# Kernel optimization log

Measured on AMD Instinct MI355X. Metric: run time of the kernel, lower is better.

The kernel has to match this reference:

```python
import jax, jax.numpy as jnp
import numpy as np

DIM = 1024
DIM_HEAD = 128
HEADS = 8
DIM_INNER = DIM_HEAD * HEADS


def setup_inputs() -> dict:
    key = jax.random.key(0)
    k_x, k_qkv, k_out = jax.random.split(key, 3)
    x = jax.random.normal(k_x, (2, 2048, DIM), dtype=jnp.float32)
    gamma = jnp.ones((DIM,), dtype=jnp.float32)
    # nn.Linear weights stored as [out, in]; init ~ U(-1/sqrt(in), 1/sqrt(in))
    w_qkv = jax.random.uniform(k_qkv, (DIM_INNER * 3, DIM), dtype=jnp.float32,
                               minval=-1.0, maxval=1.0) / np.sqrt(DIM)
    w_out = jax.random.uniform(k_out, (DIM, DIM_INNER), dtype=jnp.float32,
                               minval=-1.0, maxval=1.0) / np.sqrt(DIM_INNER)
    return {"x": x, "gamma": gamma, "w_qkv": w_qkv, "w_out": w_out}


def reference(x, gamma, w_qkv, w_out):
    scale_norm = DIM ** 0.5
    scale_attn = DIM_HEAD ** -0.5
    # RMSNorm as written: F.normalize (L2) * sqrt(dim) * gamma
    l2 = jnp.sqrt(jnp.sum(x * x, axis=-1, keepdims=True))
    xn = x / jnp.maximum(l2, 1e-12) * scale_norm * gamma
    # QKV projection: [b, n, 3*h*d]
    qkv = jnp.einsum('bnc,fc->bnf', xn, w_qkv)
    b, n, _ = qkv.shape
    qkv = qkv.reshape(b, n, 3, HEADS, DIM_HEAD)
    q, k, v = (qkv[:, :, 0], qkv[:, :, 1], qkv[:, :, 2])  # [b, n, h, d]
    q = q * scale_attn
    sim = jnp.einsum('bihd,bjhd->bhij', q, k)
    causal_mask = jnp.triu(jnp.ones((n, n), dtype=bool), k=1)
    neg = -jnp.finfo(sim.dtype).max
    sim = jnp.where(causal_mask, neg, sim)
    attn = jax.nn.softmax(sim, axis=-1)
    out = jnp.einsum('bhij,bjhd->bihd', attn, v)
    out = out.reshape(b, n, DIM_INNER)  # merge heads: b n (h d)
    return jnp.einsum('bnf,cf->bnc', out, w_out)
```

## Files before the change

kernel.cpp:

```cpp
#include <hip/hip_runtime.h>

#define SEQ 2048
#define NTOK 4096
#define DIM 1024
#define FQKV 3072
#define SC_Q (0.08838834764831843f * 1.4426950408889634f)
#define SC_NORM 32.0f

typedef short short8 __attribute__((ext_vector_type(8)));
typedef float f32x4 __attribute__((ext_vector_type(4)));
typedef float f32x16 __attribute__((ext_vector_type(16)));
typedef unsigned short u16x4 __attribute__((ext_vector_type(4)));

__device__ __forceinline__ unsigned short f2bf(float f) {
    unsigned int u = __float_as_uint(f);
    u += 0x7fffu + ((u >> 16) & 1u);
    return (unsigned short)(u >> 16);
}
__device__ __forceinline__ float bf2f(unsigned short b) {
    return __uint_as_float(((unsigned int)b) << 16);
}
__device__ __forceinline__ void gl_lds16(const void* g, void* l) {
    __builtin_amdgcn_global_load_lds((const __attribute__((address_space(1))) void*)g,
                                     (__attribute__((address_space(3))) void*)l, 16, 0, 0);
}

__global__ __launch_bounds__(256) void prep(const float* __restrict__ x,
                                            const float* __restrict__ gamma,
                                            unsigned short* __restrict__ xn,
                                            const float* __restrict__ wq,
                                            unsigned short* __restrict__ wqb,
                                            const float* __restrict__ wo,
                                            unsigned short* __restrict__ wob) {
    if (blockIdx.x < 4096) {
        int token = blockIdx.x;
        float4 v = ((const float4*)(x + (size_t)token * DIM))[threadIdx.x];
        float ss = v.x * v.x + v.y * v.y + v.z * v.z + v.w * v.w;
#pragma unroll
        for (int off = 32; off > 0; off >>= 1) ss += __shfl_down(ss, off);
        __shared__ float wsum[4];
        if ((threadIdx.x & 63) == 0) wsum[threadIdx.x >> 6] = ss;
        __syncthreads();
        float tot = wsum[0] + wsum[1] + wsum[2] + wsum[3];
        float sc = SC_NORM / fmaxf(sqrtf(tot), 1e-12f);
        float4 g = ((const float4*)gamma)[threadIdx.x];
        u16x4 o;
        o.x = f2bf(v.x * sc * g.x);
        o.y = f2bf(v.y * sc * g.y);
        o.z = f2bf(v.z * sc * g.z);
        o.w = f2bf(v.w * sc * g.w);
        ((u16x4*)(xn + (size_t)token * DIM))[threadIdx.x] = o;
    } else {
        int i = (blockIdx.x - 4096) * 256 + threadIdx.x;
        const float* w; unsigned short* o; int idx;
        if (i < 786432) { w = wq; o = wqb; idx = i; }
        else            { w = wo; o = wob; idx = i - 786432; }
        float4 v = ((const float4*)w)[idx];
        u16x4 r;
        r.x = f2bf(v.x); r.y = f2bf(v.y); r.z = f2bf(v.z); r.w = f2bf(v.w);
        ((u16x4*)o)[idx] = r;
    }
}

template<int C_MODE, int TM>
__global__ __launch_bounds__(256) void gemm_bf16(const unsigned short* __restrict__ A,
                                                 const unsigned short* __restrict__ B,
                                                 void* __restrict__ Cv,
                                                 int M, int N, int K) {
    constexpr int MF = TM / 32;
    __shared__ unsigned short As[TM * 64];
    __shared__ unsigned short Bs[128 * 64];

    int lin = blockIdx.y * gridDim.x + blockIdx.x;
    int nwg = gridDim.x * gridDim.y;
    int w = (lin & 7) * (nwg >> 3) + (lin >> 3);
    int bx = w % gridDim.x, by = w / gridDim.x;

    const int bn = bx * 128, bm = by * TM;
    const int tid = threadIdx.x, lane = tid & 63, wv = tid >> 6;
    const int wr = wv >> 1, wc = wv & 1;
    const int l15 = lane & 15, g = lane >> 4;

    f32x4 acc[MF][4] = {};

    auto stage = [&](int k0) {
#pragma unroll
        for (int ia = 0; ia < TM / 32; ++ia) {
            int ci = ia * 256 + wv * 64 + lane;
            int row = ci >> 3, cc = ci & 7;
            int co = (cc ^ (row & 7)) << 3;
            gl_lds16(A + (size_t)(bm + row) * K + k0 + co, &As[(ia * 256 + wv * 64) * 8]);
        }
#pragma unroll
        for (int ib = 0; ib < 4; ++ib) {
            int ci = ib * 256 + wv * 64 + lane;
            int row = ci >> 3, cc = ci & 7;
            int co = (cc ^ (row & 7)) << 3;
            gl_lds16(B + (size_t)(bn + row) * K + k0 + co, &Bs[(ib * 256 + wv * 64) * 8]);
        }
    };

    stage(0);
    asm volatile("s_waitcnt vmcnt(0)\ns_barrier" ::: "memory");

    for (int k0 = 0; k0 < K; k0 += 64) {
        short8 af[2][MF], bf[2][4];
#pragma unroll
        for (int ks = 0; ks < 2; ++ks) {
#pragma unroll
            for (int f = 0; f < MF; ++f) {
                int ra = wr * (TM / 2) + f * 16 + l15;
                af[ks][f] = *(const short8*)&As[ra * 64 + (((ks * 4 + g) ^ (ra & 7)) << 3)];
            }
#pragma unroll
            for (int f = 0; f < 4; ++f) {
                int rb = wc * 64 + f * 16 + l15;
                bf[ks][f] = *(const short8*)&Bs[rb * 64 + (((ks * 4 + g) ^ (rb & 7)) << 3)];
            }
        }
        asm volatile("s_waitcnt lgkmcnt(0)\ns_barrier" ::: "memory");
        if (k0 + 64 < K) stage(k0 + 64);
#pragma unroll
        for (int ks = 0; ks < 2; ++ks)
#pragma unroll
            for (int i = 0; i < MF; ++i)
#pragma unroll
                for (int j = 0; j < 4; ++j)
                    acc[i][j] = __builtin_amdgcn_mfma_f32_16x16x32_bf16(af[ks][i], bf[ks][j], acc[i][j], 0, 0, 0);
        asm volatile("s_waitcnt vmcnt(0)\ns_barrier" ::: "memory");
    }

    if (C_MODE == 0) {
        float* C = (float*)Cv;
#pragma unroll
        for (int i = 0; i < MF; ++i)
#pragma unroll
            for (int j = 0; j < 4; ++j)
#pragma unroll
                for (int v = 0; v < 4; ++v) {
                    int row = bm + wr * (TM / 2) + i * 16 + g * 4 + v;
                    int col = bn + wc * 64 + j * 16 + l15;
                    C[(size_t)row * N + col] = acc[i][j][v];
                }
    } else {
        unsigned short* C = (unsigned short*)Cv;
        float s = (bn < 1024) ? SC_Q : 1.0f;
#pragma unroll
        for (int i = 0; i < MF; ++i)
#pragma unroll
            for (int j = 0; j < 4; ++j)
#pragma unroll
                for (int v = 0; v < 4; ++v) {
                    int row = bm + wr * (TM / 2) + i * 16 + g * 4 + v;
                    int col = bn + wc * 64 + j * 16 + l15;
                    C[(size_t)row * N + col] = f2bf(acc[i][j][v] * s);
                }
    }
}

__global__ __launch_bounds__(256) void transpose_v(const unsigned short* __restrict__ qkv,
                                                   unsigned short* __restrict__ vt) {
    __shared__ unsigned short T[64][72];
    const int t0 = blockIdx.x * 64, d0 = blockIdx.y * 64, bh = blockIdx.z;
    const int b = bh >> 3, h = bh & 7;
    const int tid = threadIdx.x;
#pragma unroll
    for (int p = 0; p < 2; ++p) {
        int r = p * 32 + (tid >> 3), c = tid & 7;
        *(short8*)&T[r][c * 8] =
            *(const short8*)(qkv + (size_t)(b * SEQ + t0 + r) * FQKV + 2048 + h * 128 + d0 + c * 8);
    }
    __syncthreads();
#pragma unroll
    for (int p = 0; p < 2; ++p) {
        int d = p * 32 + (tid >> 3), c = tid & 7;
        short8 v;
#pragma unroll
        for (int j = 0; j < 8; ++j) v[j] = (short)T[c * 8 + j][d];
        *(short8*)(vt + (size_t)(bh * 128 + d0 + d) * SEQ + t0 + c * 8) = v;
    }
}

__global__ __launch_bounds__(128) void attn_mfma(const unsigned short* __restrict__ qkv,
                                                 const unsigned short* __restrict__ vt,
                                                 unsigned short* __restrict__ ao,
                                                 unsigned short* __restrict__ po,
                                                 float* __restrict__ pml) {
    __shared__ unsigned short Ks[64 * 128];
    __shared__ unsigned short Vs[128 * 64];
    __shared__ unsigned int Ps[2][32 * 32];
    const int h = blockIdx.y, b = blockIdx.z;
    const int x = blockIdx.x;
    int qblk, s, nsp;
    if (x < 30)      { qblk = 27 - x / 3;               s = x % 3;  nsp = 3; }
    else if (x < 46) { int i = x - 30; qblk = 31 - (i >> 2); s = i & 3; nsp = 4; }
    else if (x < 64) { int i = x - 46; qblk = 17 - (i >> 1); s = i & 1; nsp = 2; }
    else             { qblk = 72 - x;                   s = 0;      nsp = 1; }
    const int T = qblk + 1;
    const int jb0 = (s * T) / nsp, jb1 = ((s + 1) * T) / nsp;
    const int split = (nsp > 1);
    const int slot = ((b * 8 + h) << 6) + x;

    const int tid = threadIdx.x, lane = tid & 63, wv = tid >> 6;
    const int q = lane & 31, hi = lane >> 5;
    const int q0 = qblk * 64;
    const int qrow = q0 + wv * 32 + q;

    auto stageK = [&](int jb) {
#pragma unroll
        for (int inst = 0; inst < 8; ++inst) {
            int ci = inst * 128 + tid;
            int rowk = ci >> 4, ck = ci & 15;
            gl_lds16(qkv + (size_t)(b * SEQ + jb * 64 + rowk) * FQKV + 1024 + h * 128
                         + ((ck ^ (rowk & 7)) << 3),
                     &Ks[ci * 8]);
        }
    };
    auto stageV = [&](int jb) {
#pragma unroll
        for (int inst = 0; inst < 8; ++inst) {
            int ci = inst * 128 + tid;
            int rowv = ci >> 3, cv = ci & 7;
            gl_lds16(vt + (size_t)((b * 8 + h) * 128 + rowv) * SEQ + jb * 64
                        + ((cv ^ (rowv & 7)) << 3),
                     &Vs[ci * 8]);
        }
    };

    short8 qf[8];
    {
        const unsigned short* qb = qkv + (size_t)(b * SEQ + qrow) * FQKV + h * 128;
#pragma unroll
        for (int ks = 0; ks < 8; ++ks) qf[ks] = *(const short8*)(qb + ks * 16 + hi * 8);
    }

    float m_r = -1e30f, l_r = 0.f;
    f32x16 o[4] = {};

    stageK(jb0);
    __syncthreads();

    for (int jb = jb0; jb < jb1; ++jb) {
        stageV(jb);

        f32x16 sv[2] = {};
        __builtin_amdgcn_s_setprio(1);
#pragma unroll
        for (int ks = 0; ks < 8; ++ks) {
#pragma unroll
            for (int fi = 0; fi < 2; ++fi) {
                int rk = fi * 32 + q;
                short8 kf = *(const short8*)&Ks[rk * 128 + (((ks * 2 + hi) ^ (rk & 7)) << 3)];
                sv[fi] = __builtin_amdgcn_mfma_f32_32x32x16_bf16(kf, qf[ks], sv[fi], 0, 0, 0);
            }
        }
        __builtin_amdgcn_s_setprio(0);

        if (jb == qblk) {
#pragma unroll
            for (int fi = 0; fi < 2; ++fi)
#pragma unroll
                for (int r = 0; r < 16; ++r) {
                    int kv = jb * 64 + fi * 32 + (r & 3) + 8 * (r >> 2) + 4 * hi;
                    if (kv > qrow) sv[fi][r] = -1e30f;
                }
        }

        float mx = -1e30f;
#pragma unroll
        for (int fi = 0; fi < 2; ++fi)
#pragma unroll
            for (int r = 0; r < 16; ++r) mx = fmaxf(mx, sv[fi][r]);
        mx = fmaxf(mx, __shfl_xor(mx, 32));
        if (__any(mx - m_r > 16.0f)) {
            float Mn = fmaxf(m_r, mx);
            float alpha = exp2f(m_r - Mn);
            l_r *= alpha;
#pragma unroll
            for (int fd = 0; fd < 4; ++fd)
#pragma unroll
                for (int r = 0; r < 16; ++r) o[fd][r] *= alpha;
            m_r = Mn;
        }

        float ps = 0.f;
#pragma unroll
        for (int fi = 0; fi < 2; ++fi) {
#pragma unroll
            for (int rp = 0; rp < 8; ++rp) {
                float e0 = exp2f(sv[fi][2 * rp] - m_r);
                float e1 = exp2f(sv[fi][2 * rp + 1] - m_r);
                ps += e0 + e1;
                unsigned int pk;
                asm("v_cvt_pk_bf16_f32 %0, %1, %2" : "=v"(pk) : "v"(e0), "v"(e1));
                int kvp = (rp & 1) + ((rp >> 1) << 2) + 2 * hi + fi * 16;
                Ps[wv][q * 32 + (kvp ^ ((q & 7) << 2))] = pk;
            }
        }
        ps += __shfl_xor(ps, 32);
        l_r += ps;

        __syncthreads();
        if (jb + 1 < jb1) stageK(jb + 1);

        __builtin_amdgcn_s_setprio(1);
#pragma unroll
        for (int c = 0; c < 4; ++c) {
            short8 pb = *(const short8*)((const unsigned short*)
                            &Ps[wv][q * 32 + (((c * 8 + hi * 4)) ^ ((q & 7) << 2))]);
#pragma unroll
            for (int fd = 0; fd < 4; ++fd) {
                int rv = fd * 32 + q;
                short8 vf = *(const short8*)&Vs[rv * 64 + (((c * 2 + hi) ^ (rv & 7)) << 3)];
                o[fd] = __builtin_amdgcn_mfma_f32_32x32x16_bf16(vf, pb, o[fd], 0, 0, 0);
            }
        }
        __builtin_amdgcn_s_setprio(0);

        __syncthreads();
    }

    if (split) {
        unsigned short* od = po + (size_t)slot * 8192;
#pragma unroll
        for (int fd = 0; fd < 4; ++fd)
#pragma unroll
            for (int rp = 0; rp < 8; ++rp) {
                float e0 = o[fd][2 * rp], e1 = o[fd][2 * rp + 1];
                unsigned int pk;
                asm("v_cvt_pk_bf16_f32 %0, %1, %2" : "=v"(pk) : "v"(e0), "v"(e1));
                int d = fd * 32 + ((2 * rp) & 3) + 8 * (rp >> 1) + 4 * hi;
                *(unsigned int*)(od + (wv * 32 + q) * 128 + d) = pk;
            }
        if (hi == 0) {
            pml[(size_t)slot * 128 + wv * 32 + q] = m_r;
            pml[(size_t)slot * 128 + 64 + wv * 32 + q] = l_r;
        }
    } else {
        float inv = 1.0f / l_r;
        unsigned short* dst = ao + (size_t)(b * SEQ + qrow) * DIM + h * 128;
#pragma unroll
        for (int fd = 0; fd < 4; ++fd)
#pragma unroll
            for (int rp = 0; rp < 8; ++rp) {
                float e0 = o[fd][2 * rp] * inv, e1 = o[fd][2 * rp + 1] * inv;
                unsigned int pk;
                asm("v_cvt_pk_bf16_f32 %0, %1, %2" : "=v"(pk) : "v"(e0), "v"(e1));
                int d = fd * 32 + ((2 * rp) & 3) + 8 * (rp >> 1) + 4 * hi;
                *(unsigned int*)(dst + d) = pk;
            }
    }
}

__global__ __launch_bounds__(256) void attn_combine(const unsigned short* __restrict__ po,
                                                    const float* __restrict__ pml,
                                                    unsigned short* __restrict__ ao) {
    const int qblk = 9 + blockIdx.x, h = blockIdx.y, b = blockIdx.z;
    int base, n;
    if (qblk >= 28)      { base = 30 + (31 - qblk) * 4; n = 4; }
    else if (qblk >= 18) { base = (27 - qblk) * 3;      n = 3; }
    else                 { base = 46 + (17 - qblk) * 2; n = 2; }
    const int slot0 = ((b * 8 + h) << 6) + base;
    const int row = threadIdx.x >> 2, dp = threadIdx.x & 3;

    float M = -1e30f;
#pragma unroll
    for (int s2 = 0; s2 < 4; ++s2)
        if (s2 < n) M = fmaxf(M, pml[(size_t)(slot0 + s2) * 128 + row]);
    float denom = 0.f;
#pragma unroll
    for (int s2 = 0; s2 < 4; ++s2)
        if (s2 < n) denom += exp2f(pml[(size_t)(slot0 + s2) * 128 + row] - M)
                             * pml[(size_t)(slot0 + s2) * 128 + 64 + row];
    float inv = 1.0f / denom;

    float acc[32] = {};
#pragma unroll
    for (int s2 = 0; s2 < 4; ++s2)
        if (s2 < n) {
            float wgt = exp2f(pml[(size_t)(slot0 + s2) * 128 + row] - M) * inv;
            const unsigned short* ob = po + (size_t)(slot0 + s2) * 8192 + row * 128 + dp * 32;
#pragma unroll
            for (int j = 0; j < 4; ++j) {
                short8 pv = *(const short8*)(ob + j * 8);
#pragma unroll
                for (int e = 0; e < 8; ++e)
                    acc[j * 8 + e] += wgt * bf2f((unsigned short)pv[e]);
            }
        }

    unsigned short* dst = ao + ((size_t)(b * SEQ + qblk * 64 + row)) * DIM + h * 128 + dp * 32;
#pragma unroll
    for (int j = 0; j < 4; ++j) {
        short8 r;
#pragma unroll
        for (int e = 0; e < 8; ++e) r[e] = (short)f2bf(acc[j * 8 + e]);
        *(short8*)(dst + j * 8) = r;
    }
}

extern "C" void kernel_launch(void* const* d_in, const int* in_sizes, int n_in,
                              void* d_out, int out_size, void* d_ws, size_t ws_size,
                              hipStream_t stream) {
    const float* x     = (const float*)d_in[0];
    const float* gamma = (const float*)d_in[1];
    const float* w_qkv = (const float*)d_in[2];
    const float* w_out = (const float*)d_in[3];

    char* ws = (char*)d_ws;
    unsigned short* qkvb = (unsigned short*)ws;
    unsigned short* vtb  = (unsigned short*)(ws + 25165824);
    unsigned short* xnb  = (unsigned short*)(ws + 33554432);
    unsigned short* wqb  = (unsigned short*)(ws + 41943040);
    unsigned short* wob  = (unsigned short*)(ws + 48234496);
    unsigned short* aob  = (unsigned short*)(ws + 50331648);
    float*          pml  = (float*)(ws + 41943040);
    unsigned short* po   = (unsigned short*)d_out;

    prep<<<8192, 256, 0, stream>>>(x, gamma, xnb, w_qkv, wqb, w_out, wob);
    gemm_bf16<1, 128><<<dim3(24, 32), 256, 0, stream>>>(xnb, wqb, qkvb, NTOK, FQKV, DIM);
    transpose_v<<<dim3(32, 2, 16), 256, 0, stream>>>(qkvb, vtb);
    attn_mfma<<<dim3(73, 8, 2), 128, 0, stream>>>(qkvb, vtb, aob, po, pml);
    attn_combine<<<dim3(23, 8, 2), 256, 0, stream>>>(po, pml, aob);
    gemm_bf16<0, 64><<<dim3(8, 64), 256, 0, stream>>>(aob, wob, (float*)d_out, NTOK, DIM, DIM);
}
```

Before: 133.0 us.

## Enlarge attention query tile to 128 rows with four waves and rebalanced split-KV

The attention kernel now processes 128-query tiles with four waves per block instead of 64-query tiles with two waves. Each staged K/V tile is shared by twice as many query rows, which cuts global-to-LDS traffic per query. The split-KV schedule is rebuilt for 16 query superblocks with up to six splits, and partials overflow into the reused xn buffer. The combine kernel is adapted to match. The costs are fewer blocks in the grid, coarser load balancing, and partial causal masking applied across two diagonal blocks per wave.

Result: slower. 141.4 us (+6.3%).

```diff
diff --git a/kernel.cpp b/kernel.cpp
--- a/kernel.cpp
+++ b/kernel.cpp
@@ -181,35 +181,38 @@
     }
 }
 
-__global__ __launch_bounds__(128) void attn_mfma(const unsigned short* __restrict__ qkv,
+__global__ __launch_bounds__(256) void attn_mfma(const unsigned short* __restrict__ qkv,
                                                  const unsigned short* __restrict__ vt,
                                                  unsigned short* __restrict__ ao,
                                                  unsigned short* __restrict__ po,
+                                                 unsigned short* __restrict__ poB,
                                                  float* __restrict__ pml) {
     __shared__ unsigned short Ks[64 * 128];
     __shared__ unsigned short Vs[128 * 64];
-    __shared__ unsigned int Ps[2][32 * 32];
+    __shared__ unsigned int Ps[4][32 * 32];
     const int h = blockIdx.y, b = blockIdx.z;
     const int x = blockIdx.x;
-    int qblk, s, nsp;
-    if (x < 30)      { qblk = 27 - x / 3;               s = x % 3;  nsp = 3; }
-    else if (x < 46) { int i = x - 30; qblk = 31 - (i >> 2); s = i & 3; nsp = 4; }
-    else if (x < 64) { int i = x - 46; qblk = 17 - (i >> 1); s = i & 1; nsp = 2; }
-    else             { qblk = 72 - x;                   s = 0;      nsp = 1; }
-    const int T = qblk + 1;
+    int qsb, s, nsp;
+    if (x < 6)       { qsb = 15;            s = x;      nsp = 6; }
+    else if (x < 21) { int i = x - 6;  qsb = 14 - i / 5; s = i % 5; nsp = 5; }
+    else if (x < 33) { int i = x - 21; qsb = 11 - i / 4; s = i % 4; nsp = 4; }
+    else if (x < 42) { int i = x - 33; qsb = 8  - i / 3; s = i % 3; nsp = 3; }
+    else if (x < 48) { int i = x - 42; qsb = 5  - i / 2; s = i % 2; nsp = 2; }
+    else             { qsb = 50 - x;        s = 0;      nsp = 1; }
+    const int T = 2 * qsb + 2;
     const int jb0 = (s * T) / nsp, jb1 = ((s + 1) * T) / nsp;
     const int split = (nsp > 1);
-    const int slot = ((b * 8 + h) << 6) + x;
+    const int slot = (b * 8 + h) * 48 + x;
 
     const int tid = threadIdx.x, lane = tid & 63, wv = tid >> 6;
     const int q = lane & 31, hi = lane >> 5;
-    const int q0 = qblk * 64;
+    const int q0 = qsb * 128;
     const int qrow = q0 + wv * 32 + q;
 
     auto stageK = [&](int jb) {
 #pragma unroll
-        for (int inst = 0; inst < 8; ++inst) {
-            int ci = inst * 128 + tid;
+        for (int inst = 0; inst < 4; ++inst) {
+            int ci = inst * 256 + tid;
             int rowk = ci >> 4, ck = ci & 15;
             gl_lds16(qkv + (size_t)(b * SEQ + jb * 64 + rowk) * FQKV + 1024 + h * 128
                          + ((ck ^ (rowk & 7)) << 3),
@@ -218,8 +221,8 @@
     };
     auto stageV = [&](int jb) {
 #pragma unroll
-        for (int inst = 0; inst < 8; ++inst) {
-            int ci = inst * 128 + tid;
+        for (int inst = 0; inst < 4; ++inst) {
+            int ci = inst * 256 + tid;
             int rowv = ci >> 3, cv = ci & 7;
             gl_lds16(vt + (size_t)((b * 8 + h) * 128 + rowv) * SEQ + jb * 64
                         + ((cv ^ (rowv & 7)) << 3),
@@ -256,7 +259,7 @@
         }
         __builtin_amdgcn_s_setprio(0);
 
-        if (jb == qblk) {
+        if (jb * 64 + 63 > q0 + wv * 32) {
 #pragma unroll
             for (int fi = 0; fi < 2; ++fi)
 #pragma unroll
@@ -321,20 +324,21 @@
     }
 
     if (split) {
-        unsigned short* od = po + (size_t)slot * 8192;
+        unsigned short* od = (slot < 512) ? po + (size_t)slot * 16384
+                                          : poB + (size_t)(slot - 512) * 16384;
 #pragma unroll
         for (int fd = 0; fd < 4; ++fd)
 #pragma unroll
             for (int rp = 0; rp < 8; ++rp) {
-                float e0 = o[fd][2 * rp], e1 = o[fd][2 * rp + 1];
                 unsigned int pk;
-                asm("v_cvt_pk_bf16_f32 %0, %1, %2" : "=v"(pk) : "v"(e0), "v"(e1));
+                asm("v_cvt_pk_bf16_f32 %0, %1, %2" : "=v"(pk)
+                    : "v"(o[fd][2 * rp]), "v"(o[fd][2 * rp + 1]));
                 int d = fd * 32 + ((2 * rp) & 3) + 8 * (rp >> 1) + 4 * hi;
                 *(unsigned int*)(od + (wv * 32 + q) * 128 + d) = pk;
             }
         if (hi == 0) {
-            pml[(size_t)slot * 128 + wv * 32 + q] = m_r;
-            pml[(size_t)slot * 128 + 64 + wv * 32 + q] = l_r;
+            pml[(size_t)slot * 256 + wv * 32 + q] = m_r;
+            pml[(size_t)slot * 256 + 128 + wv * 32 + q] = l_r;
         }
     } else {
         float inv = 1.0f / l_r;
@@ -343,9 +347,9 @@
         for (int fd = 0; fd < 4; ++fd)
 #pragma unroll
             for (int rp = 0; rp < 8; ++rp) {
-                float e0 = o[fd][2 * rp] * inv, e1 = o[fd][2 * rp + 1] * inv;
                 unsigned int pk;
-                asm("v_cvt_pk_bf16_f32 %0, %1, %2" : "=v"(pk) : "v"(e0), "v"(e1));
+                asm("v_cvt_pk_bf16_f32 %0, %1, %2" : "=v"(pk)
+                    : "v"(o[fd][2 * rp] * inv), "v"(o[fd][2 * rp + 1] * inv));
                 int d = fd * 32 + ((2 * rp) & 3) + 8 * (rp >> 1) + 4 * hi;
                 *(unsigned int*)(dst + d) = pk;
             }
@@ -353,35 +357,41 @@
 }
 
 __global__ __launch_bounds__(256) void attn_combine(const unsigned short* __restrict__ po,
+                                                    const unsigned short* __restrict__ poB,
                                                     const float* __restrict__ pml,
                                                     unsigned short* __restrict__ ao) {
-    const int qblk = 9 + blockIdx.x, h = blockIdx.y, b = blockIdx.z;
+    const int qsb = 3 + blockIdx.x, h = blockIdx.y, b = blockIdx.z;
     int base, n;
-    if (qblk >= 28)      { base = 30 + (31 - qblk) * 4; n = 4; }
-    else if (qblk >= 18) { base = (27 - qblk) * 3;      n = 3; }
-    else                 { base = 46 + (17 - qblk) * 2; n = 2; }
-    const int slot0 = ((b * 8 + h) << 6) + base;
-    const int row = threadIdx.x >> 2, dp = threadIdx.x & 3;
+    if (qsb == 15)     { base = 0;                   n = 6; }
+    else if (qsb >= 12){ base = 6 + (14 - qsb) * 5;  n = 5; }
+    else if (qsb >= 9) { base = 21 + (11 - qsb) * 4; n = 4; }
+    else if (qsb >= 6) { base = 33 + (8 - qsb) * 3;  n = 3; }
+    else               { base = 42 + (5 - qsb) * 2;  n = 2; }
+    const int slot0 = (b * 8 + h) * 48 + base;
+    const int row = threadIdx.x >> 1, d0 = (threadIdx.x & 1) * 64;
 
     float M = -1e30f;
 #pragma unroll
-    for (int s2 = 0; s2 < 4; ++s2)
-        if (s2 < n) M = fmaxf(M, pml[(size_t)(slot0 + s2) * 128 + row]);
+    for (int s2 = 0; s2 < 6; ++s2)
+        if (s2 < n) M = fmaxf(M, pml[(size_t)(slot0 + s2) * 256 + row]);
     float denom = 0.f;
 #pragma unroll
-    for (int s2 = 0; s2 < 4; ++s2)
-        if (s2 < n) denom += exp2f(pml[(size_t)(slot0 + s2) * 128 + row] - M)
-                             * pml[(size_t)(slot0 + s2) * 128 + 64 + row];
+    for (int s2 = 0; s2 < 6; ++s2)
+        if (s2 < n) denom += exp2f(pml[(size_t)(slot0 + s2) * 256 + row] - M)
+                             * pml[(size_t)(slot0 + s2) * 256 + 128 + row];
     float inv = 1.0f / denom;
 
-    float acc[32] = {};
-#pragma unroll
-    for (int s2 = 0; s2 < 4; ++s2)
+    float acc[64] = {};
+#pragma unroll
+    for (int s2 = 0; s2 < 6; ++s2)
         if (s2 < n) {
-            float wgt = exp2f(pml[(size_t)(slot0 + s2) * 128 + row] - M) * inv;
-            const unsigned short* ob = po + (size_t)(slot0 + s2) * 8192 + row * 128 + dp * 32;
-#pragma unroll
-            for (int j = 0; j < 4; ++j) {
+            int sl = slot0 + s2;
+            float wgt = exp2f(pml[(size_t)sl * 256 + row] - M) * inv;
+            const unsigned short* ob = (sl < 512 ? po + (size_t)sl * 16384
+                                                 : poB + (size_t)(sl - 512) * 16384)
+                                       + row * 128 + d0;
+#pragma unroll
+            for (int j = 0; j < 8; ++j) {
                 short8 pv = *(const short8*)(ob + j * 8);
 #pragma unroll
                 for (int e = 0; e < 8; ++e)
@@ -389,9 +399,9 @@
             }
         }
 
-    unsigned short* dst = ao + ((size_t)(b * SEQ + qblk * 64 + row)) * DIM + h * 128 + dp * 32;
-#pragma unroll
-    for (int j = 0; j < 4; ++j) {
+    unsigned short* dst = ao + ((size_t)(b * SEQ + qsb * 128 + row)) * DIM + h * 128 + d0;
+#pragma unroll
+    for (int j = 0; j < 8; ++j) {
         short8 r;
 #pragma unroll
         for (int e = 0; e < 8; ++e) r[e] = (short)f2bf(acc[j * 8 + e]);
@@ -415,12 +425,13 @@
     unsigned short* wob  = (unsigned short*)(ws + 48234496);
     unsigned short* aob  = (unsigned short*)(ws + 50331648);
     float*          pml  = (float*)(ws + 41943040);
+    unsigned short* poB  = xnb;
     unsigned short* po   = (unsigned short*)d_out;
 
     prep<<<8192, 256, 0, stream>>>(x, gamma, xnb, w_qkv, wqb, w_out, wob);
     gemm_bf16<1, 128><<<dim3(24, 32), 256, 0, stream>>>(xnb, wqb, qkvb, NTOK, FQKV, DIM);
     transpose_v<<<dim3(32, 2, 16), 256, 0, stream>>>(qkvb, vtb);
-    attn_mfma<<<dim3(73, 8, 2), 128, 0, stream>>>(qkvb, vtb, aob, po, pml);
-    attn_combine<<<dim3(23, 8, 2), 256, 0, stream>>>(po, pml, aob);
+    attn_mfma<<<dim3(51, 8, 2), 256, 0, stream>>>(qkvb, vtb, aob, po, poB, pml);
+    attn_combine<<<dim3(13, 8, 2), 256, 0, stream>>>(po, poB, pml, aob);
     gemm_bf16<0, 64><<<dim3(8, 64), 256, 0, stream>>>(aob, wob, (float*)d_out, NTOK, DIM, DIM);
 }
```
